# Kernel tuning notes

Measured on AMD Instinct MI355X. Metric: run time of the kernel, lower is better.

## Reference

```python
import jax, jax.numpy as jnp
import numpy as np
from itertools import product


def _gen_exps(num_vars, degree):
    return [e for e in product(range(degree + 1), repeat=num_vars) if sum(e) <= degree]

EXPS_W = _gen_exps(4, 3)  # 35 tuples (ex, es, ey, ew)
EXPS_B = _gen_exps(2, 3)  # 10 tuples (ey, eb)


def setup_inputs() -> dict:
    key = jax.random.key(0)
    ks = jax.random.split(key, 7)
    B, D_in, D_out = 8192, 512, 512
    x = jax.random.normal(ks[0], (B, D_in), dtype=jnp.float32)
    s = jax.random.normal(ks[1], (B, D_out), dtype=jnp.float32)
    y = jax.random.normal(ks[2], (B, D_out), dtype=jnp.float32)
    w = jax.random.normal(ks[3], (D_out, D_in), dtype=jnp.float32) * 0.05
    b = jax.random.normal(ks[4], (D_out,), dtype=jnp.float32) * 0.05
    params_w = jax.random.normal(ks[5], (len(EXPS_W),), dtype=jnp.float32) * 0.1
    params_b = jax.random.normal(ks[6], (len(EXPS_B),), dtype=jnp.float32) * 0.1
    return {"x": x, "s": s, "y": y, "w": w, "b": b, "params_w": params_w, "params_b": params_b}


def _dw(x, s, y, w, params_w):
    # unique exponent powers (computed once, reused across the 35 terms)
    px = {e: x ** e for e in {t[0] for t in EXPS_W}}
    ps = {e: s ** e for e in {t[1] for t in EXPS_W}}
    py = {e: y ** e for e in {t[2] for t in EXPS_W}}
    pw = {e: w ** e for e in {t[3] for t in EXPS_W}}
    inv_B = 1.0 / x.shape[0]
    delta_w = jnp.zeros_like(w)
    for i, (ex, es, ey, ew) in enumerate(EXPS_W):
        # (y^ey * s^es).T @ x^ex  -> [out, in]
        corr = jnp.einsum("bo,bi->oi", py[ey] * ps[es], px[ex])
        delta_w = delta_w + (params_w[i] * inv_B) * corr * pw[ew]
    # bound=None -> identity; l2_reg=0.0
    return delta_w


def _db(y, b, params_b):
    py = {e: y ** e for e in {t[0] for t in EXPS_B}}
    pb = {e: b ** e for e in {t[1] for t in EXPS_B}}
    inv_B = 1.0 / y.shape[0]
    delta_b = jnp.zeros_like(b)
    for i, (ey, eb) in enumerate(EXPS_B):
        delta_b = delta_b + (params_b[i] * inv_B) * jnp.sum(py[ey], axis=0) * pb[eb]
    return delta_b


def reference(x, s, y, w, b, params_w, params_b):
    delta_w = _dw(x, s, y, w, params_w)
    delta_b = _db(y, b, params_b)
    return delta_w, delta_b
```

## Files before the change

kernel.cpp:

```cpp
#include <hip/hip_runtime.h>

#define BD 8192
#define DD 512
#define PLANE (BD * DD)
#define NPLANES 5
#define KSPLIT 32
#define NELEM (DD * DD)

typedef __attribute__((ext_vector_type(4))) float f32x4;
typedef __attribute__((ext_vector_type(8))) short short8;

__device__ __forceinline__ float polyev2(float c0, float c1, float c2, float w, float w2) {
    return c0 + c1 * w + c2 * w2;
}

__device__ __forceinline__ unsigned short f2b(float v) {
    unsigned u = __builtin_bit_cast(unsigned, v);
    u += 0x7FFFu + ((u >> 16) & 1u);
    return (unsigned short)(u >> 16);
}

__device__ __forceinline__ void gload_lds16(const unsigned short* g, unsigned short* l) {
    __builtin_amdgcn_global_load_lds((__attribute__((address_space(1))) const void*)g,
                                     (__attribute__((address_space(3))) void*)l, 16, 0, 0);
}


__device__ __forceinline__ void prep_unit(
    const float* __restrict__ x, const float* __restrict__ s,
    const float* __restrict__ y, const float* __restrict__ pw,
    unsigned short* __restrict__ pl, float* __restrict__ csp,
    const int colq, const int bt, char* L)
{
    const int t      = threadIdx.x;
    const int colL4  = (t & 15) * 4;
    const int rg     = t >> 4;
    const int kl     = rg * 4;
    const int c0     = colq * 64;
    const int r0     = bt * 64;

    const float p23 = pw[23], p24 = pw[24], p25 = pw[25], p26 = pw[26], p27 = pw[27];
    const float p28 = pw[28], p29 = pw[29], p32 = pw[32], p33 = pw[33];

    float sm[12][4];
#pragma unroll
    for (int v = 0; v < 12; ++v)
#pragma unroll
        for (int cc = 0; cc < 4; ++cc) sm[v][cc] = 0.f;

    unsigned pk[NPLANES][4][2];

#pragma unroll
    for (int j = 0; j < 4; ++j) {
        const int row = r0 + kl + j;
        const float4 xv = *(const float4*)&x[(size_t)row * DD + c0 + colL4];
        const float4 sv = *(const float4*)&s[(size_t)row * DD + c0 + colL4];
        const float4 yv = *(const float4*)&y[(size_t)row * DD + c0 + colL4];
        const float xa[4] = {xv.x, xv.y, xv.z, xv.w};
        const float sa[4] = {sv.x, sv.y, sv.z, sv.w};
        const float ya[4] = {yv.x, yv.y, yv.z, yv.w};
#pragma unroll
        for (int cc = 0; cc < 4; ++cc) {
            const float X = xa[cc], S = sa[cc], Y = ya[cc];
            const float X2 = X * X, S2 = S * S, Y2 = Y * Y, SY = S * Y;
            sm[0][cc] += X;  sm[1][cc] += X2;      sm[2][cc] += X2 * X;
            sm[3][cc] += S;  sm[4][cc] += S2;      sm[5][cc] += S2 * S;
            sm[6][cc] += Y;  sm[7][cc] += Y2;      sm[8][cc] += Y2 * Y;
            sm[9][cc] += SY; sm[10][cc] += S2 * Y; sm[11][cc] += S * Y2;
            unsigned short tv[NPLANES];
            tv[0] = f2b(p26 * S + p23 * Y + p29 * S2 + p25 * Y2 + p28 * SY);
            tv[1] = f2b(p33 * S + p32 * Y);
            tv[2] = f2b(p27 * S + p24 * Y);
            tv[3] = f2b(X);
            tv[4] = f2b(X2);
            if ((j & 1) == 0) {
#pragma unroll
                for (int p = 0; p < NPLANES; ++p) pk[p][cc][j >> 1] = (unsigned)tv[p];
            } else {
#pragma unroll
                for (int p = 0; p < NPLANES; ++p) pk[p][cc][j >> 1] |= (unsigned)tv[p] << 16;
            }
        }
    }

#pragma unroll
    for (int p = 0; p < NPLANES; ++p) {
#pragma unroll
        for (int cc = 0; cc < 4; ++cc) {
            const int colL = colL4 + cc;
            const int addr = p * 8192 + colL * 128 + (((kl >> 3) ^ (colL & 7)) << 4) + ((kl & 4) << 1);
            uint2 u; u.x = pk[p][cc][0]; u.y = pk[p][cc][1];
            *(uint2*)&L[addr] = u;
        }
    }
    __syncthreads();

    {
        char* gbase = (char*)pl;
        const size_t blockByte = ((size_t)bt * DD + c0) * 128;
#pragma unroll
        for (int u = 0; u < 10; ++u) {
            const int byteoff = u * 4096 + t * 16;
            const int p = byteoff >> 13;
            const int within = byteoff & 8191;
            *(uint4*)(gbase + ((size_t)p * PLANE) * 2 + blockByte + within) =
                *(const uint4*)&L[byteoff];
        }
    }
    __syncthreads();

#pragma unroll
    for (int v = 0; v < 12; ++v)
#pragma unroll
        for (int cc = 0; cc < 4; ++cc) {
            sm[v][cc] += __shfl_xor(sm[v][cc], 16, 64);
            sm[v][cc] += __shfl_xor(sm[v][cc], 32, 64);
        }
    float* R = (float*)L;
    const int wv = t >> 6, ln = t & 63;
    if (ln < 16) {
#pragma unroll
        for (int v = 0; v < 12; ++v)
#pragma unroll
            for (int cc = 0; cc < 4; ++cc)
                R[(wv * 16 + ln) * 48 + v * 4 + cc] = sm[v][cc];
    }
    __syncthreads();
    if (t < 16) {
        const int blk = bt * 8 + colq;
#pragma unroll
        for (int v = 0; v < 12; ++v)
#pragma unroll
            for (int cc = 0; cc < 4; ++cc) {
                float a = R[(0 * 16 + t) * 48 + v * 4 + cc]
                        + R[(1 * 16 + t) * 48 + v * 4 + cc]
                        + R[(2 * 16 + t) * 48 + v * 4 + cc]
                        + R[(3 * 16 + t) * 48 + v * 4 + cc];
                csp[((size_t)blk * 12 + v) * 64 + t * 4 + cc] = a;
            }
    }
}

__global__ __launch_bounds__(256, 3) void prep3_kernel(
    const float* __restrict__ x, const float* __restrict__ s,
    const float* __restrict__ y, const float* __restrict__ pw,
    unsigned short* __restrict__ pl, float* __restrict__ csp)
{
    __shared__ __align__(16) char L[5 * 8192];
    prep_unit(x, s, y, pw, pl, csp, blockIdx.x, blockIdx.y, L);
}

__global__ __launch_bounds__(256) void reduce_cs_kernel(
    const float* __restrict__ csp, float* __restrict__ cs)
{
    const int u = blockIdx.x * 256 + threadIdx.x;
    if (u < 12 * DD) {
        const int v = u >> 9;
        const int c = u & 511;
        const int colq = c >> 6, cl = c & 63;
        float acc = 0.f;
        for (int bt = 0; bt < 128; ++bt)
            acc += csp[((size_t)(bt * 8 + colq) * 12 + v) * 64 + cl];
        cs[v * DD + c] = acc;
    }
}

__device__ __forceinline__ void do_tile(
    const unsigned short* __restrict__ A, const unsigned short* __restrict__ B,
    int wo, int wi, int l15, int g4, f32x4 (&acc)[4][4])
{
#pragma unroll
    for (int ss = 0; ss < 2; ++ss) {
        short8 af[4], bf[4];
#pragma unroll
        for (int m = 0; m < 4; ++m) {
            const int r = wo + m * 16 + l15;
            af[m] = *(const short8*)((const char*)A + (r << 7) + ((((ss << 2) + g4) ^ (r & 7)) << 4));
        }
#pragma unroll
        for (int n = 0; n < 4; ++n) {
            const int r = wi + n * 16 + l15;
            bf[n] = *(const short8*)((const char*)B + (r << 7) + ((((ss << 2) + g4) ^ (r & 7)) << 4));
        }
#pragma unroll
        for (int m = 0; m < 4; ++m)
#pragma unroll
            for (int n = 0; n < 4; ++n)
                acc[m][n] = __builtin_amdgcn_mfma_f32_16x16x32_bf16(af[m], bf[n], acc[m][n], 0, 0, 0);
    }
}

__global__ __launch_bounds__(256, 2) void gemm_kernel(
    const unsigned short* __restrict__ pl, const float* __restrict__ w,
    float* __restrict__ part)
{
    __shared__ unsigned short lds[4][8192];
    unsigned short* ldsp = &lds[0][0];

    const int t    = threadIdx.x;
    const int lane = t & 63;
    const int wid  = t >> 6;
    const int bid  = blockIdx.x;
    const int ks   = (bid & 7) + ((bid >> 7) << 3);
    const int tile = (bid >> 3) & 15;
    const int tileI = tile & 3;
    const int tileO = tile >> 2;
    const int wo = (wid >> 1) * 64, wi = (wid & 1) * 64;
    const int l15 = lane & 15, g4 = lane >> 4;

    const unsigned short* Am = pl + (size_t)(ks < 16 ? 0 : 1) * PLANE;
    const unsigned short* Bm = pl + (size_t)(ks < 16 ? 3 : 4) * PLANE;
    const unsigned short* Aw = pl + (size_t)2 * PLANE;
    const unsigned short* Bx = pl + (size_t)3 * PLANE;
    const int btm0 = (ks & 15) * 8;
    const int btw0 = ks * 4;

    f32x4 accM[4][4], accW[4][4];
#pragma unroll
    for (int m = 0; m < 4; ++m)
#pragma unroll
        for (int n = 0; n < 4; ++n) { accM[m][n] = (f32x4)0.f; accW[m][n] = (f32x4)0.f; }

    auto Abase = [&](int j) -> const unsigned short* {
        return (j < 8) ? Am + ((size_t)(btm0 + j) * DD + tileO * 128) * 64
                       : Aw + ((size_t)(btw0 + j - 8) * DD + tileO * 128) * 64;
    };
    auto Bbase = [&](int j) -> const unsigned short* {
        return (j < 8) ? Bm + ((size_t)(btm0 + j) * DD + tileI * 128) * 64
                       : Bx + ((size_t)(btw0 + j - 8) * DD + tileI * 128) * 64;
    };
    auto stage = [&](const unsigned short* Ag, const unsigned short* Bg, int buf) {
        unsigned short* La = ldsp + (buf * 2 + 0) * 8192;
        unsigned short* Lb = ldsp + (buf * 2 + 1) * 8192;
#pragma unroll
        for (int c = 0; c < 4; ++c) {
            gload_lds16(Ag + c * 2048 + t * 8, La + c * 2048 + wid * 512);
            gload_lds16(Bg + c * 2048 + t * 8, Lb + c * 2048 + wid * 512);
        }
    };

    stage(Abase(0), Bbase(0), 0);
    __syncthreads();
#pragma unroll 1
    for (int j = 0; j < 8; ++j) {
        const int cur = j & 1;
        stage(Abase(j + 1), Bbase(j + 1), cur ^ 1);
        do_tile(ldsp + (cur * 2 + 0) * 8192, ldsp + (cur * 2 + 1) * 8192, wo, wi, l15, g4, accM);
        __syncthreads();
    }
#pragma unroll 1
    for (int j = 8; j < 12; ++j) {
        const int cur = j & 1;
        if (j < 11) stage(Abase(j + 1), Bbase(j + 1), cur ^ 1);
        do_tile(ldsp + (cur * 2 + 0) * 8192, ldsp + (cur * 2 + 1) * 8192, wo, wi, l15, g4, accW);
        __syncthreads();
    }

    float* pout = part + (size_t)ks * NELEM;
#pragma unroll
    for (int m = 0; m < 4; ++m) {
        const int o = tileO * 128 + wo + m * 16 + g4 * 4;
#pragma unroll
        for (int n = 0; n < 4; ++n) {
            const int i = tileI * 128 + wi + n * 16 + l15;
#pragma unroll
            for (int r = 0; r < 4; ++r) {
                const float wv = w[(size_t)(o + r) * DD + i];
                pout[(size_t)(o + r) * DD + i] = accM[m][n][r] + wv * accW[m][n][r];
            }
        }
    }
}

__device__ __forceinline__ void deltab_store(
    const int o, const float* __restrict__ bvec, const float* __restrict__ pb,
    const float* __restrict__ cs, float* __restrict__ out)
{
    const float bv = bvec[o];
    const float b2 = bv * bv, b3 = b2 * bv;
    const float invB = 1.0f / (float)BD;
    float acc = (float)BD * (pb[0] + pb[1] * bv + pb[2] * b2 + pb[3] * b3);
    acc += cs[6 * DD + o] * (pb[4] + pb[5] * bv + pb[6] * b2);
    acc += cs[7 * DD + o] * (pb[7] + pb[8] * bv);
    acc += cs[8 * DD + o] * pb[9];
    out[DD * DD + o] = invB * acc;
}

__global__ __launch_bounds__(256) void reduce_rank1_kernel(
    const float* __restrict__ part, const float* __restrict__ w,
    const float* __restrict__ pw, const float* __restrict__ cs,
    const float* __restrict__ bvec, const float* __restrict__ pb,
    float* __restrict__ out)
{
    const int t   = threadIdx.x;
    const int bid = blockIdx.x;
    const int idx = (bid * 256 + t) * 4;
    const int o   = idx >> 9;
    const int i0  = idx & 511;

    float4 g = {0.f, 0.f, 0.f, 0.f};
#pragma unroll
    for (int ks = 0; ks < KSPLIT; ++ks) {
        const float4 p = *(const float4*)&part[(size_t)ks * NELEM + idx];
        g.x += p.x; g.y += p.y; g.z += p.z; g.w += p.w;
    }
    const float4 wv4 = *(const float4*)&w[idx];

    const float csY1 = cs[6 * DD + o], csY2 = cs[7 * DD + o], csY3 = cs[8 * DD + o];
    const float csS1 = cs[3 * DD + o], csS2 = cs[4 * DD + o], csS3 = cs[5 * DD + o];
    const float csSY = cs[9 * DD + o], csS2Y = cs[10 * DD + o], csSY2 = cs[11 * DD + o];
    const float4 csX1 = *(const float4*)&cs[0 * DD + i0];
    const float4 csX2 = *(const float4*)&cs[1 * DD + i0];
    const float4 csX3 = *(const float4*)&cs[2 * DD + i0];

    const float ga[4]   = {g.x, g.y, g.z, g.w};
    const float wa[4]   = {wv4.x, wv4.y, wv4.z, wv4.w};
    const float cx1[4]  = {csX1.x, csX1.y, csX1.z, csX1.w};
    const float cx2[4]  = {csX2.x, csX2.y, csX2.z, csX2.w};
    const float cx3[4]  = {csX3.x, csX3.y, csX3.z, csX3.w};

    float4 res;
    float ra[4];
#pragma unroll
    for (int l = 0; l < 4; ++l) {
        const float wv = wa[l];
        const float w2 = wv * wv, w3 = w2 * wv;
        float acc = (float)BD * (pw[0] + pw[1] * wv + pw[2] * w2 + pw[3] * w3);
        acc += cx1[l] * polyev2(pw[20], pw[21], pw[22], wv, w2);
        acc += cx2[l] * (pw[30] + pw[31] * wv);
        acc += cx3[l] * pw[34];
        acc += csY1 * polyev2(pw[4],  pw[5],  pw[6],  wv, w2);
        acc += csY2 * (pw[7] + pw[8] * wv);
        acc += csY3 * pw[9];
        acc += csS1 * polyev2(pw[10], pw[11], pw[12], wv, w2);
        acc += csSY * (pw[13] + pw[14] * wv);
        acc += csSY2 * pw[15];
        acc += csS2 * (pw[16] + pw[17] * wv);
        acc += csS2Y * pw[18];
        acc += csS3 * pw[19];
        ra[l] = (1.0f / (float)BD) * (ga[l] + acc);
    }
    res.x = ra[0]; res.y = ra[1]; res.z = ra[2]; res.w = ra[3];
    *(float4*)&out[idx] = res;

    if (bid == 0) {
        deltab_store(t,       bvec, pb, cs, out);
        deltab_store(t + 256, bvec, pb, cs, out);
    }
}

extern "C" void kernel_launch(void* const* d_in, const int* in_sizes, int n_in,
                              void* d_out, int out_size, void* d_ws, size_t ws_size,
                              hipStream_t stream) {
    const float* x  = (const float*)d_in[0];
    const float* s  = (const float*)d_in[1];
    const float* y  = (const float*)d_in[2];
    const float* w  = (const float*)d_in[3];
    const float* b  = (const float*)d_in[4];
    const float* pw = (const float*)d_in[5];
    const float* pb = (const float*)d_in[6];
    float* out = (float*)d_out;

    const size_t planeBytes = (size_t)PLANE * 2 * NPLANES;
    const size_t partBytes  = (size_t)KSPLIT * NELEM * sizeof(float);
    const size_t cspBytes   = (size_t)1024 * 12 * 64 * sizeof(float);
    const size_t csBytes    = 12 * DD * sizeof(float);
    if (ws_size < planeBytes + partBytes + cspBytes + csBytes) return;

    unsigned short* pl = (unsigned short*)d_ws;
    float* part = (float*)((char*)d_ws + planeBytes);
    float* csp  = (float*)((char*)d_ws + planeBytes + partBytes);
    float* cs   = (float*)((char*)d_ws + planeBytes + partBytes + cspBytes);

    prep3_kernel<<<dim3(8, 128), 256, 0, stream>>>(x, s, y, pw, pl, csp);
    reduce_cs_kernel<<<24, 256, 0, stream>>>(csp, cs);
    gemm_kernel<<<512, 256, 0, stream>>>(pl, w, part);
    reduce_rank1_kernel<<<256, 256, 0, stream>>>(part, w, pw, cs, b, pb, out);
}
```

Baseline: 140.0 us.

## Fuse bf16 plane preparation and column sums into the split-K GEMM kernel

The separate prep kernel that wrote five bf16 planes to global memory is removed. The GEMM kernel now loads fp32 x/s/y tiles directly into registers, computes the polynomial combinations and converts them to bf16 into padded LDS, and accumulates per-column moment sums on selected tiles. It software-pipelines global loads against the MFMA work with a double buffer. This removes the plane write and re-read traffic and one launch. In exchange each GEMM block recomputes conversions redundantly across tiles, reads fp32 instead of bf16, and no longer uses async global-to-LDS loads.

```diff
diff --git a/kernel.cpp b/kernel.cpp
--- a/kernel.cpp
+++ b/kernel.cpp
@@ -2,8 +2,6 @@
 
 #define BD 8192
 #define DD 512
-#define PLANE (BD * DD)
-#define NPLANES 5
 #define KSPLIT 32
 #define NELEM (DD * DD)
 
@@ -20,182 +18,14 @@
     return (unsigned short)(u >> 16);
 }
 
-__device__ __forceinline__ void gload_lds16(const unsigned short* g, unsigned short* l) {
-    __builtin_amdgcn_global_load_lds((__attribute__((address_space(1))) const void*)g,
-                                     (__attribute__((address_space(3))) void*)l, 16, 0, 0);
-}
-
-
-__device__ __forceinline__ void prep_unit(
+
+__global__ __launch_bounds__(256, 2) void gemm2_kernel(
     const float* __restrict__ x, const float* __restrict__ s,
-    const float* __restrict__ y, const float* __restrict__ pw,
-    unsigned short* __restrict__ pl, float* __restrict__ csp,
-    const int colq, const int bt, char* L)
+    const float* __restrict__ y, const float* __restrict__ w,
+    const float* __restrict__ pw,
+    float* __restrict__ part, float* __restrict__ csp)
 {
-    const int t      = threadIdx.x;
-    const int colL4  = (t & 15) * 4;
-    const int rg     = t >> 4;
-    const int kl     = rg * 4;
-    const int c0     = colq * 64;
-    const int r0     = bt * 64;
-
-    const float p23 = pw[23], p24 = pw[24], p25 = pw[25], p26 = pw[26], p27 = pw[27];
-    const float p28 = pw[28], p29 = pw[29], p32 = pw[32], p33 = pw[33];
-
-    float sm[12][4];
-#pragma unroll
-    for (int v = 0; v < 12; ++v)
-#pragma unroll
-        for (int cc = 0; cc < 4; ++cc) sm[v][cc] = 0.f;
-
-    unsigned pk[NPLANES][4][2];
-
-#pragma unroll
-    for (int j = 0; j < 4; ++j) {
-        const int row = r0 + kl + j;
-        const float4 xv = *(const float4*)&x[(size_t)row * DD + c0 + colL4];
-        const float4 sv = *(const float4*)&s[(size_t)row * DD + c0 + colL4];
-        const float4 yv = *(const float4*)&y[(size_t)row * DD + c0 + colL4];
-        const float xa[4] = {xv.x, xv.y, xv.z, xv.w};
-        const float sa[4] = {sv.x, sv.y, sv.z, sv.w};
-        const float ya[4] = {yv.x, yv.y, yv.z, yv.w};
-#pragma unroll
-        for (int cc = 0; cc < 4; ++cc) {
-            const float X = xa[cc], S = sa[cc], Y = ya[cc];
-            const float X2 = X * X, S2 = S * S, Y2 = Y * Y, SY = S * Y;
-            sm[0][cc] += X;  sm[1][cc] += X2;      sm[2][cc] += X2 * X;
-            sm[3][cc] += S;  sm[4][cc] += S2;      sm[5][cc] += S2 * S;
-            sm[6][cc] += Y;  sm[7][cc] += Y2;      sm[8][cc] += Y2 * Y;
-            sm[9][cc] += SY; sm[10][cc] += S2 * Y; sm[11][cc] += S * Y2;
-            unsigned short tv[NPLANES];
-            tv[0] = f2b(p26 * S + p23 * Y + p29 * S2 + p25 * Y2 + p28 * SY);
-            tv[1] = f2b(p33 * S + p32 * Y);
-            tv[2] = f2b(p27 * S + p24 * Y);
-            tv[3] = f2b(X);
-            tv[4] = f2b(X2);
-            if ((j & 1) == 0) {
-#pragma unroll
-                for (int p = 0; p < NPLANES; ++p) pk[p][cc][j >> 1] = (unsigned)tv[p];
-            } else {
-#pragma unroll
-                for (int p = 0; p < NPLANES; ++p) pk[p][cc][j >> 1] |= (unsigned)tv[p] << 16;
-            }
-        }
-    }
-
-#pragma unroll
-    for (int p = 0; p < NPLANES; ++p) {
-#pragma unroll
-        for (int cc = 0; cc < 4; ++cc) {
-            const int colL = colL4 + cc;
-            const int addr = p * 8192 + colL * 128 + (((kl >> 3) ^ (colL & 7)) << 4) + ((kl & 4) << 1);
-            uint2 u; u.x = pk[p][cc][0]; u.y = pk[p][cc][1];
-            *(uint2*)&L[addr] = u;
-        }
-    }
-    __syncthreads();
-
-    {
-        char* gbase = (char*)pl;
-        const size_t blockByte = ((size_t)bt * DD + c0) * 128;
-#pragma unroll
-        for (int u = 0; u < 10; ++u) {
-            const int byteoff = u * 4096 + t * 16;
-            const int p = byteoff >> 13;
-            const int within = byteoff & 8191;
-            *(uint4*)(gbase + ((size_t)p * PLANE) * 2 + blockByte + within) =
-                *(const uint4*)&L[byteoff];
-        }
-    }
-    __syncthreads();
-
-#pragma unroll
-    for (int v = 0; v < 12; ++v)
-#pragma unroll
-        for (int cc = 0; cc < 4; ++cc) {
-            sm[v][cc] += __shfl_xor(sm[v][cc], 16, 64);
-            sm[v][cc] += __shfl_xor(sm[v][cc], 32, 64);
-        }
-    float* R = (float*)L;
-    const int wv = t >> 6, ln = t & 63;
-    if (ln < 16) {
-#pragma unroll
-        for (int v = 0; v < 12; ++v)
-#pragma unroll
-            for (int cc = 0; cc < 4; ++cc)
-                R[(wv * 16 + ln) * 48 + v * 4 + cc] = sm[v][cc];
-    }
-    __syncthreads();
-    if (t < 16) {
-        const int blk = bt * 8 + colq;
-#pragma unroll
-        for (int v = 0; v < 12; ++v)
-#pragma unroll
-            for (int cc = 0; cc < 4; ++cc) {
-                float a = R[(0 * 16 + t) * 48 + v * 4 + cc]
-                        + R[(1 * 16 + t) * 48 + v * 4 + cc]
-                        + R[(2 * 16 + t) * 48 + v * 4 + cc]
-                        + R[(3 * 16 + t) * 48 + v * 4 + cc];
-                csp[((size_t)blk * 12 + v) * 64 + t * 4 + cc] = a;
-            }
-    }
-}
-
-__global__ __launch_bounds__(256, 3) void prep3_kernel(
-    const float* __restrict__ x, const float* __restrict__ s,
-    const float* __restrict__ y, const float* __restrict__ pw,
-    unsigned short* __restrict__ pl, float* __restrict__ csp)
-{
-    __shared__ __align__(16) char L[5 * 8192];
-    prep_unit(x, s, y, pw, pl, csp, blockIdx.x, blockIdx.y, L);
-}
-
-__global__ __launch_bounds__(256) void reduce_cs_kernel(
-    const float* __restrict__ csp, float* __restrict__ cs)
-{
-    const int u = blockIdx.x * 256 + threadIdx.x;
-    if (u < 12 * DD) {
-        const int v = u >> 9;
-        const int c = u & 511;
-        const int colq = c >> 6, cl = c & 63;
-        float acc = 0.f;
-        for (int bt = 0; bt < 128; ++bt)
-            acc += csp[((size_t)(bt * 8 + colq) * 12 + v) * 64 + cl];
-        cs[v * DD + c] = acc;
-    }
-}
-
-__device__ __forceinline__ void do_tile(
-    const unsigned short* __restrict__ A, const unsigned short* __restrict__ B,
-    int wo, int wi, int l15, int g4, f32x4 (&acc)[4][4])
-{
-#pragma unroll
-    for (int ss = 0; ss < 2; ++ss) {
-        short8 af[4], bf[4];
-#pragma unroll
-        for (int m = 0; m < 4; ++m) {
-            const int r = wo + m * 16 + l15;
-            af[m] = *(const short8*)((const char*)A + (r << 7) + ((((ss << 2) + g4) ^ (r & 7)) << 4));
-        }
-#pragma unroll
-        for (int n = 0; n < 4; ++n) {
-            const int r = wi + n * 16 + l15;
-            bf[n] = *(const short8*)((const char*)B + (r << 7) + ((((ss << 2) + g4) ^ (r & 7)) << 4));
-        }
-#pragma unroll
-        for (int m = 0; m < 4; ++m)
-#pragma unroll
-            for (int n = 0; n < 4; ++n)
-                acc[m][n] = __builtin_amdgcn_mfma_f32_16x16x32_bf16(af[m], bf[n], acc[m][n], 0, 0, 0);
-    }
-}
-
-__global__ __launch_bounds__(256, 2) void gemm_kernel(
-    const unsigned short* __restrict__ pl, const float* __restrict__ w,
-    float* __restrict__ part)
-{
-    __shared__ unsigned short lds[4][8192];
-    unsigned short* ldsp = &lds[0][0];
+    __shared__ short lds[2][2][128 * 40];
 
     const int t    = threadIdx.x;
     const int lane = t & 63;
@@ -208,12 +38,15 @@
     const int wo = (wid >> 1) * 64, wi = (wid & 1) * 64;
     const int l15 = lane & 15, g4 = lane >> 4;
 
-    const unsigned short* Am = pl + (size_t)(ks < 16 ? 0 : 1) * PLANE;
-    const unsigned short* Bm = pl + (size_t)(ks < 16 ? 3 : 4) * PLANE;
-    const unsigned short* Aw = pl + (size_t)2 * PLANE;
-    const unsigned short* Bx = pl + (size_t)3 * PLANE;
-    const int btm0 = (ks & 15) * 8;
-    const int btw0 = ks * 4;
+    const int q    = lane >> 4;
+    const int cp   = (lane & 15) * 2;
+    const int lcA  = wid * 32 + cp;
+    const int colA = tileO * 128 + lcA;
+    const int colB = tileI * 128 + lcA;
+
+    const float p23 = pw[23], p24 = pw[24], p25 = pw[25], p26 = pw[26], p27 = pw[27];
+    const float p28 = pw[28], p29 = pw[29], p32 = pw[32], p33 = pw[33];
+    const bool half2 = (ks >= 16);
 
     f32x4 accM[4][4], accW[4][4];
 #pragma unroll
@@ -221,39 +54,98 @@
 #pragma unroll
         for (int n = 0; n < 4; ++n) { accM[m][n] = (f32x4)0.f; accW[m][n] = (f32x4)0.f; }
 
-    auto Abase = [&](int j) -> const unsigned short* {
-        return (j < 8) ? Am + ((size_t)(btm0 + j) * DD + tileO * 128) * 64
-                       : Aw + ((size_t)(btw0 + j - 8) * DD + tileO * 128) * 64;
+    float smA[2][9];
+    float smB[2][3];
+#pragma unroll
+    for (int j = 0; j < 2; ++j) {
+#pragma unroll
+        for (int v = 0; v < 9; ++v) smA[j][v] = 0.f;
+#pragma unroll
+        for (int v = 0; v < 3; ++v) smB[j][v] = 0.f;
+    }
+
+    float2 rs[8], ry[8], rx[8];
+
+    auto LOAD = [&](int R0) {
+#pragma unroll
+        for (int p = 0; p < 8; ++p) {
+            const int r = R0 + q * 8 + p;
+            rs[p] = *(const float2*)&s[(size_t)r * DD + colA];
+            ry[p] = *(const float2*)&y[(size_t)r * DD + colA];
+            rx[p] = *(const float2*)&x[(size_t)r * DD + colB];
+        }
     };
-    auto Bbase = [&](int j) -> const unsigned short* {
-        return (j < 8) ? Bm + ((size_t)(btm0 + j) * DD + tileI * 128) * 64
-                       : Bx + ((size_t)(btw0 + j - 8) * DD + tileI * 128) * 64;
+
+    auto WRITE = [&](int buf, int mode, bool bx2, bool sumA, bool sumB) {
+        unsigned pa[2][4], pb[2][4];
+#pragma unroll
+        for (int p = 0; p < 8; ++p) {
+            const float sv[2] = { rs[p].x, rs[p].y };
+            const float yv[2] = { ry[p].x, ry[p].y };
+            const float xv[2] = { rx[p].x, rx[p].y };
+#pragma unroll
+            for (int j = 0; j < 2; ++j) {
+                const float S = sv[j], Y = yv[j], X = xv[j];
+                const float S2 = S * S, Y2 = Y * Y;
+                float av;
+                if (mode == 0)      av = p26 * S + p23 * Y + p29 * S2 + p25 * Y2 + p28 * (S * Y);
+                else if (mode == 1) av = p33 * S + p32 * Y;
+                else                av = p27 * S + p24 * Y;
+                const float X2 = X * X;
+                const float bv = bx2 ? X2 : X;
+                const unsigned short ab = f2b(av), bb = f2b(bv);
+                if ((p & 1) == 0) { pa[j][p >> 1] = (unsigned)ab; pb[j][p >> 1] = (unsigned)bb; }
+                else              { pa[j][p >> 1] |= (unsigned)ab << 16; pb[j][p >> 1] |= (unsigned)bb << 16; }
+                if (sumA) {
+                    smA[j][0] += S;     smA[j][1] += S2;     smA[j][2] += S2 * S;
+                    smA[j][3] += Y;     smA[j][4] += Y2;     smA[j][5] += Y2 * Y;
+                    smA[j][6] += S * Y; smA[j][7] += S2 * Y; smA[j][8] += S * Y2;
+                }
+                if (sumB) { smB[j][0] += X; smB[j][1] += X2; smB[j][2] += X2 * X; }
+            }
+        }
+#pragma unroll
+        for (int j = 0; j < 2; ++j) {
+            uint4 ua; ua.x = pa[j][0]; ua.y = pa[j][1]; ua.z = pa[j][2]; ua.w = pa[j][3];
+            uint4 ub; ub.x = pb[j][0]; ub.y = pb[j][1]; ub.z = pb[j][2]; ub.w = pb[j][3];
+            *(uint4*)&lds[buf][0][(lcA + j) * 40 + q * 8] = ua;
+            *(uint4*)&lds[buf][1][(lcA + j) * 40 + q * 8] = ub;
+        }
     };
-    auto stage = [&](const unsigned short* Ag, const unsigned short* Bg, int buf) {
-        unsigned short* La = ldsp + (buf * 2 + 0) * 8192;
-        unsigned short* Lb = ldsp + (buf * 2 + 1) * 8192;
-#pragma unroll
-        for (int c = 0; c < 4; ++c) {
-            gload_lds16(Ag + c * 2048 + t * 8, La + c * 2048 + wid * 512);
-            gload_lds16(Bg + c * 2048 + t * 8, Lb + c * 2048 + wid * 512);
-        }
+
+    auto MFMA = [&](int buf, f32x4 (&acc)[4][4]) {
+        short8 af[4], bf[4];
+#pragma unroll
+        for (int m = 0; m < 4; ++m)
+            af[m] = *(const short8*)&lds[buf][0][(wo + m * 16 + l15) * 40 + g4 * 8];
+#pragma unroll
+        for (int n = 0; n < 4; ++n)
+            bf[n] = *(const short8*)&lds[buf][1][(wi + n * 16 + l15) * 40 + g4 * 8];
+#pragma unroll
+        for (int m = 0; m < 4; ++m)
+#pragma unroll
+            for (int n = 0; n < 4; ++n)
+                acc[m][n] = __builtin_amdgcn_mfma_f32_16x16x32_bf16(af[m], bf[n], acc[m][n], 0, 0, 0);
     };
 
-    stage(Abase(0), Bbase(0), 0);
-    __syncthreads();
+    const int Rm = (ks & 15) * 512;
+    const int modeM = half2 ? 1 : 0;
+
+    LOAD(Rm);
 #pragma unroll 1
-    for (int j = 0; j < 8; ++j) {
-        const int cur = j & 1;
-        stage(Abase(j + 1), Bbase(j + 1), cur ^ 1);
-        do_tile(ldsp + (cur * 2 + 0) * 8192, ldsp + (cur * 2 + 1) * 8192, wo, wi, l15, g4, accM);
+    for (int st = 0; st < 24; ++st) {
+        const int buf = st & 1;
+        const bool merged = st < 16;
+        const bool sumA = !half2 && merged && ((st >> 2) == tileI);
+        const bool sumB = !half2 && merged && ((st >> 2) == tileO);
+        WRITE(buf, merged ? modeM : 2, merged && half2, sumA, sumB);
+        if (st < 23) {
+            const int nst = st + 1;
+            const int R0n = (nst < 16) ? (Rm + nst * 32) : (ks * 256 + (nst - 16) * 32);
+            LOAD(R0n);
+        }
         __syncthreads();
-    }
-#pragma unroll 1
-    for (int j = 8; j < 12; ++j) {
-        const int cur = j & 1;
-        if (j < 11) stage(Abase(j + 1), Bbase(j + 1), cur ^ 1);
-        do_tile(ldsp + (cur * 2 + 0) * 8192, ldsp + (cur * 2 + 1) * 8192, wo, wi, l15, g4, accW);
-        __syncthreads();
+        MFMA(buf, merged ? accM : accW);
     }
 
     float* pout = part + (size_t)ks * NELEM;
@@ -269,6 +161,50 @@
                 pout[(size_t)(o + r) * DD + i] = accM[m][n][r] + wv * accW[m][n][r];
             }
         }
+    }
+
+    if (!half2) {
+#pragma unroll
+        for (int j = 0; j < 2; ++j) {
+#pragma unroll
+            for (int v = 0; v < 9; ++v) {
+                smA[j][v] += __shfl_xor(smA[j][v], 16, 64);
+                smA[j][v] += __shfl_xor(smA[j][v], 32, 64);
+            }
+#pragma unroll
+            for (int v = 0; v < 3; ++v) {
+                smB[j][v] += __shfl_xor(smB[j][v], 16, 64);
+                smB[j][v] += __shfl_xor(smB[j][v], 32, 64);
+            }
+        }
+        if (lane < 16) {
+            const int slotA = ks * 4 + tileI;
+            const int slotB = ks * 4 + tileO;
+#pragma unroll
+            for (int j = 0; j < 2; ++j) {
+#pragma unroll
+                for (int v = 0; v < 9; ++v)
+                    csp[((size_t)slotA * 12 + 3 + v) * DD + colA + j] = smA[j][v];
+#pragma unroll
+                for (int v = 0; v < 3; ++v)
+                    csp[((size_t)slotB * 12 + v) * DD + colB + j] = smB[j][v];
+            }
+        }
+    }
+}
+
+__global__ __launch_bounds__(256) void reduce_cs_kernel(
+    const float* __restrict__ csp, float* __restrict__ cs)
+{
+    const int u = blockIdx.x * 256 + threadIdx.x;
+    if (u < 12 * DD) {
+        const int v = u >> 9;
+        const int c = u & 511;
+        float acc = 0.f;
+#pragma unroll 4
+        for (int slot = 0; slot < 64; ++slot)
+            acc += csp[((size_t)slot * 12 + v) * DD + c];
+        cs[v * DD + c] = acc;
     }
 }
 
@@ -313,11 +249,11 @@
     const float4 csX2 = *(const float4*)&cs[1 * DD + i0];
     const float4 csX3 = *(const float4*)&cs[2 * DD + i0];
 
-    const float ga[4]   = {g.x, g.y, g.z, g.w};
-    const float wa[4]   = {wv4.x, wv4.y, wv4.z, wv4.w};
-    const float cx1[4]  = {csX1.x, csX1.y, csX1.z, csX1.w};
-    const float cx2[4]  = {csX2.x, csX2.y, csX2.z, csX2.w};
-    const float cx3[4]  = {csX3.x, csX3.y, csX3.z, csX3.w};
+    const float ga[4]  = {g.x, g.y, g.z, g.w};
+    const float wa[4]  = {wv4.x, wv4.y, wv4.z, wv4.w};
+    const float cx1[4] = {csX1.x, csX1.y, csX1.z, csX1.w};
+    const float cx2[4] = {csX2.x, csX2.y, csX2.z, csX2.w};
+    const float cx3[4] = {csX3.x, csX3.y, csX3.z, csX3.w};
 
     float4 res;
     float ra[4];
@@ -361,19 +297,16 @@
     const float* pb = (const float*)d_in[6];
     float* out = (float*)d_out;
 
-    const size_t planeBytes = (size_t)PLANE * 2 * NPLANES;
-    const size_t partBytes  = (size_t)KSPLIT * NELEM * sizeof(float);
-    const size_t cspBytes   = (size_t)1024 * 12 * 64 * sizeof(float);
-    const size_t csBytes    = 12 * DD * sizeof(float);
-    if (ws_size < planeBytes + partBytes + cspBytes + csBytes) return;
-
-    unsigned short* pl = (unsigned short*)d_ws;
-    float* part = (float*)((char*)d_ws + planeBytes);
-    float* csp  = (float*)((char*)d_ws + planeBytes + partBytes);
-    float* cs   = (float*)((char*)d_ws + planeBytes + partBytes + cspBytes);
-
-    prep3_kernel<<<dim3(8, 128), 256, 0, stream>>>(x, s, y, pw, pl, csp);
+    const size_t partBytes = (size_t)KSPLIT * NELEM * sizeof(float);
+    const size_t cspBytes  = (size_t)64 * 12 * DD * sizeof(float);
+    const size_t csBytes   = 12 * DD * sizeof(float);
+    if (ws_size < partBytes + cspBytes + csBytes) return;
+
+    float* part = (float*)d_ws;
+    float* csp  = (float*)((char*)d_ws + partBytes);
+    float* cs   = (float*)((char*)d_ws + partBytes + cspBytes);
+
+    gemm2_kernel<<<512, 256, 0, stream>>>(x, s, y, w, pw, part, csp);
     reduce_cs_kernel<<<24, 256, 0, stream>>>(csp, cs);
-    gemm_kernel<<<512, 256, 0, stream>>>(pl, w, part);
     reduce_rank1_kernel<<<256, 256, 0, stream>>>(part, w, pw, cs, b, pb, out);
 }
```

Result: slower. 207.3 us (+48.1%).
